# Optimization experiments

Measured on AMD Instinct MI355X. Metric: run time of the kernel, lower is better.

Reference implementation:

```python
import jax, jax.numpy as jnp
import numpy as np

# dims (match init_kwargs / input_specs)
B, T, IN, H, OUT, BR = 128, 250, 700, 512, 20, 4
VTH, DT, WARMUP = 1.0, 1.0, 10


@jax.custom_vjp
def spike_fn(v):
    # Heaviside spike with surrogate gradient (ActFun_adp style)
    return (v > 0.0).astype(v.dtype)

def _spike_fwd(v):
    return spike_fn(v), v

def _spike_bwd(v, g):
    gamma, lens = 0.5, 0.5  # gaussian surrogate
    return (g * gamma * jnp.exp(-v * v / (2.0 * lens * lens)),)

spike_fn.defvjp(_spike_fwd, _spike_bwd)


def make_mask(rng, out_dim, in_dim, branch):
    # each output neuron's branch j sees a disjoint random slice of inputs
    m = np.zeros((out_dim * branch, in_dim), np.float32)
    seg = in_dim // branch
    for i in range(out_dim):
        perm = rng.permutation(in_dim)
        for j in range(branch):
            m[i * branch + j, perm[j * seg:(j + 1) * seg]] = 1.0
    return jnp.asarray(m)


def setup_inputs() -> dict:
    key = jax.random.key(0)
    ks = jax.random.split(key, 12)
    rng = np.random.default_rng(0)
    lim1 = 1.0 / np.sqrt(IN)
    lim2 = 1.0 / np.sqrt(H)
    return {
        "x": jax.random.uniform(ks[0], (B, T, IN), dtype=jnp.float32),
        "W1": jax.random.uniform(ks[1], (H * BR, IN), minval=-lim1, maxval=lim1),
        "b1": jax.random.uniform(ks[2], (H * BR,), minval=-lim1, maxval=lim1),
        "tau_m1": jax.random.uniform(ks[3], (H,), minval=0.0, maxval=4.0),
        "tau_n1": jax.random.uniform(ks[4], (H, BR), minval=0.0, maxval=4.0),
        "mask1": make_mask(rng, H, IN, BR),
        "W2": jax.random.uniform(ks[5], (H * BR, H), minval=-lim2, maxval=lim2),
        "b2": jax.random.uniform(ks[6], (H * BR,), minval=-lim2, maxval=lim2),
        "tau_m2": jax.random.uniform(ks[7], (H,), minval=0.0, maxval=4.0),
        "tau_n2": jax.random.uniform(ks[8], (H, BR), minval=0.0, maxval=4.0),
        "mask2": make_mask(rng, H, H, BR),
        "Wo": jax.random.uniform(ks[9], (OUT, H), minval=-lim2, maxval=lim2),
        "bo": jax.random.uniform(ks[10], (OUT,), minval=-lim2, maxval=lim2),
        "tau_mo": jax.random.uniform(ks[11], (OUT,), minval=0.0, maxval=4.0),
    }


def reference(x, W1, b1, tau_m1, tau_n1, mask1, W2, b2, tau_m2, tau_n2, mask2, Wo, bo, tau_mo):
    beta1 = jax.nn.sigmoid(tau_n1)   # [H,BR] dendritic decay
    alpha1 = jax.nn.sigmoid(tau_m1)  # [H]   membrane decay
    beta2 = jax.nn.sigmoid(tau_n2)
    alpha2 = jax.nn.sigmoid(tau_m2)
    alpha_o = jax.nn.sigmoid(tau_mo)  # [OUT]
    Wm1 = W1 * mask1  # dendritic branch connectivity mask
    Wm2 = W2 * mask2
    Bsz = x.shape[0]
    Hd, Br = tau_n1.shape
    Od = tau_mo.shape[0]

    init = (jnp.zeros((Bsz, Hd, Br)), jnp.zeros((Bsz, Hd)), jnp.zeros((Bsz, Hd)),
            jnp.zeros((Bsz, Hd, Br)), jnp.zeros((Bsz, Hd)), jnp.zeros((Bsz, Hd)),
            jnp.zeros((Bsz, Od)))

    def step(c, xt):
        d1, m1, s1, d2, m2, s2, mo = c
        # layer 1: dendritic filter then LIF membrane with soft reset
        d1 = beta1 * d1 + (1.0 - beta1) * (xt @ Wm1.T + b1).reshape(Bsz, Hd, Br)
        m1 = m1 * alpha1 + (1.0 - alpha1) * DT * d1.sum(-1) - VTH * s1
        s1 = spike_fn(m1 - VTH)
        # layer 2
        d2 = beta2 * d2 + (1.0 - beta2) * (s1 @ Wm2.T + b2).reshape(Bsz, Hd, Br)
        m2 = m2 * alpha2 + (1.0 - alpha2) * DT * d2.sum(-1) - VTH * s2
        s2 = spike_fn(m2 - VTH)
        # leaky readout integrator (no spiking)
        mo = mo * alpha_o + (1.0 - alpha_o) * DT * (s2 @ Wo.T + bo)
        return (d1, m1, s1, d2, m2, s2, mo), jax.nn.softmax(mo, axis=1)

    _, ys = jax.lax.scan(step, init, jnp.swapaxes(x, 0, 1))  # ys: [T,B,OUT]
    # readout_mode == 'sum_softmax': skip steps i <= warmup_steps, sum the rest
    return ys[WARMUP + 1:].sum(0)
```

## Files before the change

### kernel.cpp

```cpp
#include <hip/hip_runtime.h>
#include <math.h>
#include <stdint.h>

#define B_    128
#define T_    250
#define IN_   700
#define INP_  704
#define H_    512
#define OUT_  20
#define BR_   4
#define HB_   2048
#define WARM_ 10
#define VTH_  1.0f

typedef __attribute__((ext_vector_type(8))) _Float16 half8;
typedef __attribute__((ext_vector_type(4))) float f32x4;
typedef __attribute__((ext_vector_type(4))) int i32x4;
typedef const __attribute__((address_space(1))) void* gptr_t;
typedef __attribute__((address_space(3))) void* lptr_t;

__global__ __launch_bounds__(256)
void w1prep_kernel(const float* __restrict__ W, const float* __restrict__ M,
                   _Float16* __restrict__ w0, _Float16* __restrict__ w1) {
    int i = blockIdx.x * 256 + threadIdx.x;
    if (i >= HB_ * INP_) return;
    int r = i / INP_, c = i - r * INP_;
    float v = (c < IN_) ? W[(size_t)r * IN_ + c] * M[(size_t)r * IN_ + c] : 0.f;
    _Float16 h0 = (_Float16)v;
    w0[i] = h0;
    w1[i] = (_Float16)(v - (float)h0);
}

__global__ __launch_bounds__(256)
void w2prep_kernel(const float* __restrict__ W, const float* __restrict__ M,
                   int8_t* __restrict__ p2, int8_t* __restrict__ p1,
                   int8_t* __restrict__ p0) {
    int i = blockIdx.x * 256 + threadIdx.x;
    if (i >= HB_ * H_) return;
    float v = W[i] * M[i];
    int q = (int)lrintf(v * 67108864.f);
    int b0 = (int)(int8_t)(q & 0xFF);  q = (q - b0) >> 8;
    int b1 = (int)(int8_t)(q & 0xFF);  int b2 = (q - b1) >> 8;
    p0[i] = (int8_t)b0; p1[i] = (int8_t)b1; p2[i] = (int8_t)b2;
}

__global__ __launch_bounds__(256)
void woprep_kernel(const float* __restrict__ Wo, _Float16* __restrict__ wo0,
                   _Float16* __restrict__ wo1) {
    int i = blockIdx.x * 256 + threadIdx.x;
    if (i >= 32 * H_) return;
    int n = i >> 9;
    float v = (n < OUT_) ? Wo[(size_t)n * H_ + (i & (H_ - 1))] : 0.f;
    _Float16 h0 = (_Float16)v;
    wo0[i] = h0;
    wo1[i] = (_Float16)(v - (float)h0);
}

__global__ __launch_bounds__(256)
void convx_kernel(const float* __restrict__ x, _Float16* __restrict__ x0,
                  _Float16* __restrict__ x1, int t0, int tc, int ntot) {
    int i = blockIdx.x * 256 + threadIdx.x;
    if (i >= ntot) return;
    int r = i / INP_, c = i - r * INP_;
    int bb = r / tc, tl = r - bb * tc;
    float v = (c < IN_) ? x[((size_t)bb * T_ + t0 + tl) * IN_ + c] : 0.f;
    _Float16 h0 = (_Float16)v;
    x0[i] = h0;
    x1[i] = (_Float16)(v - (float)h0);
}

__global__ void zero_kernel(float* __restrict__ p, int n4) {
    int i = blockIdx.x * blockDim.x + threadIdx.x;
    if (i < n4) ((float4*)p)[i] = make_float4(0.f, 0.f, 0.f, 0.f);
}

__global__ __launch_bounds__(256)
void l1_gemm_kernel(const _Float16* __restrict__ x0, const _Float16* __restrict__ x1,
                    const _Float16* __restrict__ w0, const _Float16* __restrict__ w1,
                    const float* __restrict__ bias, float* __restrict__ C) {
    __shared__ alignas(16) _Float16 A0s[128 * 32];
    __shared__ alignas(16) _Float16 A1s[128 * 32];
    __shared__ alignas(16) _Float16 B0s[128 * 32];
    __shared__ alignas(16) _Float16 B1s[128 * 32];
    const int tid  = threadIdx.x;
    const int wave = tid >> 6, lane = tid & 63;
    const int bm = blockIdx.x * 128, bn = blockIdx.y * 128;

    const int    srow  = tid >> 2;
    const int    skoff = (tid & 3) * 8;
    const size_t aoff0 = (size_t)(bm + srow) * INP_ + skoff;
    const size_t aoff1 = aoff0 + (size_t)64 * INP_;
    const size_t boff0 = (size_t)(bn + srow) * INP_ + skoff;
    const size_t boff1 = boff0 + (size_t)64 * INP_;
    const int lo0 = wave * 512, lo1 = 2048 + wave * 512;

    const int wm = wave & 1, wn = wave >> 1;
    const int fr = lane & 15;
    const int fk = (lane >> 4) * 8;

    f32x4 acc[4][4] = {};

    for (int kt = 0; kt < INP_ / 32; kt++) {
        const int k0 = kt * 32;
        __builtin_amdgcn_global_load_lds((gptr_t)(x0 + aoff0 + k0), (lptr_t)(A0s + lo0), 16, 0, 0);
        __builtin_amdgcn_global_load_lds((gptr_t)(x0 + aoff1 + k0), (lptr_t)(A0s + lo1), 16, 0, 0);
        __builtin_amdgcn_global_load_lds((gptr_t)(x1 + aoff0 + k0), (lptr_t)(A1s + lo0), 16, 0, 0);
        __builtin_amdgcn_global_load_lds((gptr_t)(x1 + aoff1 + k0), (lptr_t)(A1s + lo1), 16, 0, 0);
        __builtin_amdgcn_global_load_lds((gptr_t)(w0 + boff0 + k0), (lptr_t)(B0s + lo0), 16, 0, 0);
        __builtin_amdgcn_global_load_lds((gptr_t)(w0 + boff1 + k0), (lptr_t)(B0s + lo1), 16, 0, 0);
        __builtin_amdgcn_global_load_lds((gptr_t)(w1 + boff0 + k0), (lptr_t)(B1s + lo0), 16, 0, 0);
        __builtin_amdgcn_global_load_lds((gptr_t)(w1 + boff1 + k0), (lptr_t)(B1s + lo1), 16, 0, 0);
        __syncthreads();

        half8 a0[4], a1[4], b0[4], b1[4];
#pragma unroll
        for (int mi = 0; mi < 4; mi++)
            a0[mi] = *(const half8*)&A0s[(wm * 64 + mi * 16 + fr) * 32 + fk];
#pragma unroll
        for (int ni = 0; ni < 4; ni++)
            b0[ni] = *(const half8*)&B0s[(wn * 64 + ni * 16 + fr) * 32 + fk];
#pragma unroll
        for (int mi = 0; mi < 4; mi++)
#pragma unroll
            for (int ni = 0; ni < 4; ni++)
                acc[mi][ni] = __builtin_amdgcn_mfma_f32_16x16x32_f16(a0[mi], b0[ni], acc[mi][ni], 0, 0, 0);
#pragma unroll
        for (int ni = 0; ni < 4; ni++)
            b1[ni] = *(const half8*)&B1s[(wn * 64 + ni * 16 + fr) * 32 + fk];
#pragma unroll
        for (int mi = 0; mi < 4; mi++)
#pragma unroll
            for (int ni = 0; ni < 4; ni++)
                acc[mi][ni] = __builtin_amdgcn_mfma_f32_16x16x32_f16(a0[mi], b1[ni], acc[mi][ni], 0, 0, 0);
#pragma unroll
        for (int mi = 0; mi < 4; mi++)
            a1[mi] = *(const half8*)&A1s[(wm * 64 + mi * 16 + fr) * 32 + fk];
#pragma unroll
        for (int mi = 0; mi < 4; mi++)
#pragma unroll
            for (int ni = 0; ni < 4; ni++)
                acc[mi][ni] = __builtin_amdgcn_mfma_f32_16x16x32_f16(a1[mi], b0[ni], acc[mi][ni], 0, 0, 0);
        __syncthreads();
    }

    const int cc = lane & 15;
    const int cr = (lane >> 4) * 4;
#pragma unroll
    for (int ni = 0; ni < 4; ni++) {
        const int gc = bn + wn * 64 + ni * 16 + cc;
        const float bv = bias[gc];
#pragma unroll
        for (int mi = 0; mi < 4; mi++) {
            const int gr = bm + wm * 64 + mi * 16 + cr;
            float* cp = C + (size_t)gr * HB_ + gc;
#pragma unroll
            for (int r = 0; r < 4; r++) cp[(size_t)r * HB_] = acc[mi][ni][r] + bv;
        }
    }
}

__global__ __launch_bounds__(256)
void mfma_i8_gemm_kernel(const int8_t* __restrict__ A,
                         const int8_t* __restrict__ p2, const int8_t* __restrict__ p1,
                         const int8_t* __restrict__ p0,
                         const float* __restrict__ bias, float* __restrict__ C) {
    __shared__ alignas(16) int8_t As[128 * 64];
    __shared__ alignas(16) int8_t Bs[128 * 64];
    const int tid  = threadIdx.x;
    const int wave = tid >> 6, lane = tid & 63;
    const int bm = blockIdx.x * 128, bn = blockIdx.y * 128;

    const int    srow  = tid >> 2;
    const int    skoff = (tid & 3) * 16;
    const size_t aoff0 = (size_t)(bm + srow) * H_ + skoff;
    const size_t aoff1 = aoff0 + (size_t)64 * H_;
    const size_t boff0 = (size_t)(bn + srow) * H_ + skoff;
    const size_t boff1 = boff0 + (size_t)64 * H_;
    lptr_t lA0 = (lptr_t)(As + wave * 1024);
    lptr_t lA1 = (lptr_t)(As + 4096 + wave * 1024);
    lptr_t lB0 = (lptr_t)(Bs + wave * 1024);
    lptr_t lB1 = (lptr_t)(Bs + 4096 + wave * 1024);

    const int wm = wave & 1, wn = wave >> 1;
    const int fr = lane & 15;
    const int fk = (lane >> 4) * 16;

    const int8_t* planes[3] = {p2, p1, p0};
    i32x4 acc[4][4] = {};

#pragma unroll
    for (int s = 0; s < 3; s++) {
        if (s) {
#pragma unroll
            for (int mi = 0; mi < 4; mi++)
#pragma unroll
                for (int ni = 0; ni < 4; ni++) acc[mi][ni] *= 256;
        }
        const int8_t* pw = planes[s];
        for (int kt = 0; kt < H_ / 64; kt++) {
            const int k0 = kt * 64;
            __builtin_amdgcn_global_load_lds((gptr_t)(A  + aoff0 + k0), lA0, 16, 0, 0);
            __builtin_amdgcn_global_load_lds((gptr_t)(A  + aoff1 + k0), lA1, 16, 0, 0);
            __builtin_amdgcn_global_load_lds((gptr_t)(pw + boff0 + k0), lB0, 16, 0, 0);
            __builtin_amdgcn_global_load_lds((gptr_t)(pw + boff1 + k0), lB1, 16, 0, 0);
            __syncthreads();

            i32x4 af[4], bf[4];
#pragma unroll
            for (int mi = 0; mi < 4; mi++)
                af[mi] = *(const i32x4*)&As[(wm * 64 + mi * 16 + fr) * 64 + fk];
#pragma unroll
            for (int ni = 0; ni < 4; ni++)
                bf[ni] = *(const i32x4*)&Bs[(wn * 64 + ni * 16 + fr) * 64 + fk];
#pragma unroll
            for (int mi = 0; mi < 4; mi++)
#pragma unroll
                for (int ni = 0; ni < 4; ni++)
                    acc[mi][ni] = __builtin_amdgcn_mfma_i32_16x16x64_i8(
                        af[mi], bf[ni], acc[mi][ni], 0, 0, 0);
            __syncthreads();
        }
    }

    const float scale = 1.f / 67108864.f;
    const int cc = lane & 15;
    const int cr = (lane >> 4) * 4;
#pragma unroll
    for (int ni = 0; ni < 4; ni++) {
        const int gc = bn + wn * 64 + ni * 16 + cc;
        const float bv = bias[gc];
#pragma unroll
        for (int mi = 0; mi < 4; mi++) {
            const int gr = bm + wm * 64 + mi * 16 + cr;
            float* cp = C + (size_t)gr * HB_ + gc;
#pragma unroll
            for (int r = 0; r < 4; r++)
                cp[(size_t)r * HB_] = (float)acc[mi][ni][r] * scale + bv;
        }
    }
}

#define SCAN_BODY(SPIKE_STORE)                                                  \
    int idx = blockIdx.x * 256 + threadIdx.x;                                   \
    int b = idx >> 9;                                                           \
    int h = idx & (H_ - 1);                                                     \
    float alpha = 1.f / (1.f + expf(-tau_m[h]));                                \
    float4 tn = ((const float4*)tau_n)[h];                                      \
    float4 beta;                                                                \
    beta.x = 1.f / (1.f + expf(-tn.x));                                         \
    beta.y = 1.f / (1.f + expf(-tn.y));                                         \
    beta.z = 1.f / (1.f + expf(-tn.z));                                         \
    beta.w = 1.f / (1.f + expf(-tn.w));                                         \
    float4 d = ((const float4*)dst)[idx];                                       \
    float m = mst[idx];                                                         \
    float sp = spst[idx];                                                       \
    const float* cp = cur + (size_t)b * tc * HB_ + h * BR_;                     \
    for (int t = 0; t < tc; t++) {                                              \
        float4 c = *(const float4*)cp;                                          \
        cp += HB_;                                                              \
        d.x = beta.x * d.x + (1.f - beta.x) * c.x;                              \
        d.y = beta.y * d.y + (1.f - beta.y) * c.y;                              \
        d.z = beta.z * d.z + (1.f - beta.z) * c.z;                              \
        d.w = beta.w * d.w + (1.f - beta.w) * c.w;                              \
        float s4 = ((d.x + d.y) + d.z) + d.w;                                   \
        m = m * alpha + (1.f - alpha) * s4 - VTH_ * sp;                         \
        sp = (m > VTH_) ? 1.f : 0.f;                                            \
        SPIKE_STORE;                                                            \
    }                                                                           \
    ((float4*)dst)[idx] = d;                                                    \
    mst[idx] = m;                                                               \
    spst[idx] = sp;

__global__ __launch_bounds__(256)
void scan_i8_kernel(const float* __restrict__ cur, float* __restrict__ dst,
                    float* __restrict__ mst, float* __restrict__ spst,
                    int8_t* __restrict__ sout, const float* __restrict__ tau_m,
                    const float* __restrict__ tau_n, int tc) {
    SCAN_BODY(sout[((size_t)b * tc + t) * H_ + h] = (int8_t)(m > VTH_))
}

__global__ __launch_bounds__(256)
void scan_f16_kernel(const float* __restrict__ cur, float* __restrict__ dst,
                     float* __restrict__ mst, float* __restrict__ spst,
                     _Float16* __restrict__ sout, const float* __restrict__ tau_m,
                     const float* __restrict__ tau_n, int tc) {
    SCAN_BODY(sout[((size_t)b * tc + t) * H_ + h] = (_Float16)sp)
}

__global__ __launch_bounds__(256)
void rdot_mfma_kernel(const _Float16* __restrict__ s2c, const _Float16* __restrict__ wo0,
                      const _Float16* __restrict__ wo1, const float* __restrict__ bo,
                      float* __restrict__ curo, int t0, int tc) {
    __shared__ alignas(16) _Float16 As[128 * 32];
    __shared__ alignas(16) _Float16 B0s[32 * 32];
    __shared__ alignas(16) _Float16 B1s[32 * 32];
    const int tid  = threadIdx.x;
    const int wave = tid >> 6, lane = tid & 63;
    const int bm = blockIdx.x * 128;

    const int    srow  = tid >> 2;
    const int    skoff = (tid & 3) * 8;
    const size_t aoff0 = (size_t)(bm + srow) * H_ + skoff;
    const size_t aoff1 = aoff0 + (size_t)64 * H_;
    lptr_t lA0 = (lptr_t)(As + wave * 512);
    lptr_t lA1 = (lptr_t)(As + 2048 + wave * 512);
    const _Float16* bsrc = (wave < 2) ? wo0 : wo1;
    const int bw = wave & 1;
    const size_t boff = (size_t)(bw * 16 + (lane >> 2)) * H_ + (lane & 3) * 8;
    lptr_t lB = (lptr_t)(((wave < 2) ? B0s : B1s) + bw * 512);

    const int fr = lane & 15;
    const int fk = (lane >> 4) * 8;

    f32x4 acc[2][2] = {};

    for (int kt = 0; kt < H_ / 32; kt++) {
        const int k0 = kt * 32;
        __builtin_amdgcn_global_load_lds((gptr_t)(s2c + aoff0 + k0), lA0, 16, 0, 0);
        __builtin_amdgcn_global_load_lds((gptr_t)(s2c + aoff1 + k0), lA1, 16, 0, 0);
        __builtin_amdgcn_global_load_lds((gptr_t)(bsrc + boff + k0), lB, 16, 0, 0);
        __syncthreads();

        half8 af[2], b0[2], b1[2];
#pragma unroll
        for (int mi = 0; mi < 2; mi++)
            af[mi] = *(const half8*)&As[(wave * 32 + mi * 16 + fr) * 32 + fk];
#pragma unroll
        for (int ni = 0; ni < 2; ni++) {
            b0[ni] = *(const half8*)&B0s[(ni * 16 + fr) * 32 + fk];
            b1[ni] = *(const half8*)&B1s[(ni * 16 + fr) * 32 + fk];
        }
#pragma unroll
        for (int mi = 0; mi < 2; mi++)
#pragma unroll
            for (int ni = 0; ni < 2; ni++) {
                acc[mi][ni] = __builtin_amdgcn_mfma_f32_16x16x32_f16(af[mi], b0[ni], acc[mi][ni], 0, 0, 0);
                acc[mi][ni] = __builtin_amdgcn_mfma_f32_16x16x32_f16(af[mi], b1[ni], acc[mi][ni], 0, 0, 0);
            }
        __syncthreads();
    }

    const int cc = lane & 15;
    const int cr = (lane >> 4) * 4;
#pragma unroll
    for (int ni = 0; ni < 2; ni++) {
        const int gc = ni * 16 + cc;
        if (gc < OUT_) {
            const float bv = bo[gc];
#pragma unroll
            for (int mi = 0; mi < 2; mi++) {
#pragma unroll
                for (int r = 0; r < 4; r++) {
                    const int gr = bm + wave * 32 + mi * 16 + cr + r;
                    const int bb = gr / tc, tl = gr - bb * tc;
                    curo[((size_t)bb * T_ + t0 + tl) * OUT_ + gc] = acc[mi][ni][r] + bv;
                }
            }
        }
    }
}

#define RT_SEG 12
#define RT_LEN 21

__global__ __launch_bounds__(256)
void readout_kernel(const float* __restrict__ curo, const float* __restrict__ tau_mo,
                    float* __restrict__ out) {
    __shared__ float moS[T_ * OUT_];
    __shared__ float segA[RT_SEG][OUT_];
    __shared__ float segU[RT_SEG][OUT_];
    __shared__ float pre[RT_SEG][OUT_];
    __shared__ float accS[OUT_];
    const int b = blockIdx.x;
    const int tid = threadIdx.x;
    const float* cb = curo + (size_t)b * T_ * OUT_;

    const int o = tid % OUT_;
    const int sg = tid / OUT_;
    const float ao = 1.f / (1.f + expf(-tau_mo[o]));

    if (tid < RT_SEG * OUT_) {
        int t0 = sg * RT_LEN;
        int t1 = min(T_, t0 + RT_LEN);
        float u = 0.f, Ap = 1.f;
        for (int t = t0; t < t1; t++) {
            u = ao * u + (1.f - ao) * cb[t * OUT_ + o];
            Ap *= ao;
        }
        segU[sg][o] = u; segA[sg][o] = Ap;
    }
    if (tid < OUT_) accS[tid] = 0.f;
    __syncthreads();
    if (tid < OUT_) {
        float m = 0.f;
        for (int s = 0; s < RT_SEG; s++) {
            pre[s][tid] = m;
            m = segA[s][tid] * m + segU[s][tid];
        }
    }
    __syncthreads();
    if (tid < RT_SEG * OUT_) {
        int t0 = sg * RT_LEN;
        int t1 = min(T_, t0 + RT_LEN);
        float m = pre[sg][o];
        for (int t = t0; t < t1; t++) {
            m = ao * m + (1.f - ao) * cb[t * OUT_ + o];
            moS[t * OUT_ + o] = m;
        }
    }
    __syncthreads();
    if (tid >= WARM_ + 1 && tid < T_) {
        int t = tid;
        float mx = -3.0e38f;
#pragma unroll
        for (int o2 = 0; o2 < OUT_; o2++) mx = fmaxf(mx, moS[t * OUT_ + o2]);
        float es[OUT_]; float se = 0.f;
#pragma unroll
        for (int o2 = 0; o2 < OUT_; o2++) {
            float e = expf(moS[t * OUT_ + o2] - mx);
            es[o2] = e; se += e;
        }
        float inv = 1.f / se;
#pragma unroll
        for (int o2 = 0; o2 < OUT_; o2++) atomicAdd(&accS[o2], es[o2] * inv);
    }
    __syncthreads();
    if (tid < OUT_) out[(size_t)b * OUT_ + tid] = accS[tid];
}

extern "C" void kernel_launch(void* const* d_in, const int* in_sizes, int n_in,
                              void* d_out, int out_size, void* d_ws, size_t ws_size,
                              hipStream_t stream) {
    const float* x      = (const float*)d_in[0];
    const float* W1     = (const float*)d_in[1];
    const float* b1     = (const float*)d_in[2];
    const float* tau_m1 = (const float*)d_in[3];
    const float* tau_n1 = (const float*)d_in[4];
    const float* mask1  = (const float*)d_in[5];
    const float* W2     = (const float*)d_in[6];
    const float* b2     = (const float*)d_in[7];
    const float* tau_m2 = (const float*)d_in[8];
    const float* tau_n2 = (const float*)d_in[9];
    const float* mask2  = (const float*)d_in[10];
    const float* Wo     = (const float*)d_in[11];
    const float* bo     = (const float*)d_in[12];
    const float* tau_mo = (const float*)d_in[13];
    float* out = (float*)d_out;

    const size_t fixedB = (size_t)18 * 1024 * 1024;
    int ncs;  int tcs[3];
    if (ws_size >= fixedB + (size_t)250 * 1605632) { ncs = 1; tcs[0] = 250; }
    else if (ws_size >= fixedB + (size_t)125 * 1605632) { ncs = 2; tcs[0] = tcs[1] = 125; }
    else { ncs = 3; tcs[0] = 100; tcs[1] = 100; tcs[2] = 50; }
    const int tcm = tcs[0];

    char* p = (char*)d_ws;
    auto alloc = [&](size_t bytes) { char* r = p; p += (bytes + 255) & ~(size_t)255; return r; };
    _Float16* w10 = (_Float16*)alloc((size_t)HB_ * INP_ * 2);
    _Float16* w11 = (_Float16*)alloc((size_t)HB_ * INP_ * 2);
    int8_t*   q2  = (int8_t*)alloc((size_t)HB_ * H_);
    int8_t*   q1  = (int8_t*)alloc((size_t)HB_ * H_);
    int8_t*   q0  = (int8_t*)alloc((size_t)HB_ * H_);
    _Float16* wo0 = (_Float16*)alloc((size_t)32 * H_ * 2);
    _Float16* wo1 = (_Float16*)alloc((size_t)32 * H_ * 2);
    _Float16* xc0 = (_Float16*)alloc((size_t)B_ * tcm * INP_ * 2);
    _Float16* xc1 = (_Float16*)alloc((size_t)B_ * tcm * INP_ * 2);
    int8_t*   s1c = (int8_t*)alloc((size_t)B_ * tcm * H_);
    _Float16* s2c = (_Float16*)alloc((size_t)B_ * tcm * H_ * 2);
    float* cur    = (float*)alloc((size_t)B_ * tcm * HB_ * 4);
    float* curo   = (float*)alloc((size_t)B_ * T_ * OUT_ * 4);
    float* st     = (float*)alloc((size_t)786432 * 4);
    float* d1  = st;
    float* m1  = d1 + (size_t)B_ * H_ * BR_;
    float* sp1 = m1 + (size_t)B_ * H_;
    float* d2  = sp1 + (size_t)B_ * H_;
    float* m2  = d2 + (size_t)B_ * H_ * BR_;
    float* sp2 = m2 + (size_t)B_ * H_;

    w1prep_kernel<<<(HB_ * INP_ + 255) / 256, 256, 0, stream>>>(W1, mask1, w10, w11);
    w2prep_kernel<<<(HB_ * H_ + 255) / 256, 256, 0, stream>>>(W2, mask2, q2, q1, q0);
    woprep_kernel<<<(32 * H_ + 255) / 256, 256, 0, stream>>>(Wo, wo0, wo1);
    zero_kernel<<<(786432 / 4 + 255) / 256, 256, 0, stream>>>(st, 786432 / 4);

    int t0 = 0;
    for (int c = 0; c < ncs; c++) {
        const int tc = tcs[c];
        const int M = B_ * tc;
        dim3 gg(tc, HB_ / 128);
        convx_kernel<<<(M * INP_ + 255) / 256, 256, 0, stream>>>(x, xc0, xc1, t0, tc, M * INP_);
        l1_gemm_kernel<<<gg, 256, 0, stream>>>(xc0, xc1, w10, w11, b1, cur);
        scan_i8_kernel<<<B_ * H_ / 256, 256, 0, stream>>>(cur, d1, m1, sp1, s1c, tau_m1, tau_n1, tc);
        mfma_i8_gemm_kernel<<<gg, 256, 0, stream>>>(s1c, q2, q1, q0, b2, cur);
        scan_f16_kernel<<<B_ * H_ / 256, 256, 0, stream>>>(cur, d2, m2, sp2, s2c, tau_m2, tau_n2, tc);
        rdot_mfma_kernel<<<tc, 256, 0, stream>>>(s2c, wo0, wo1, bo, curo, t0, tc);
        t0 += tc;
    }
    readout_kernel<<<B_, 256, 0, stream>>>(curo, tau_mo, out);
}
```

Baseline: 925.5 us.

## Switch GEMMs to 32x32 MFMA tiles, swap grid order, alias spike buffers

Both the fp16 split-precision layer-1 GEMM and the int8 three-plane layer-2 GEMM move from 16x16 MFMA instructions to 32x32 ones (32x32x16 f16 and 32x32x32 i8). Each wave now holds a 2x2 grid of 16-register accumulators instead of 4x4 small ones, which is meant to cut instruction issue and LDS fragment reads per flop. The grid is transposed so the N dimension varies fastest, letting consecutive blocks share the same activation rows in cache. The workspace thresholds change, and in the single-chunk case the spike buffers reuse the converted-x buffers to save memory, which relies on those buffers no longer being needed at that point.

After: 851.8 us. 1.09x faster.

```diff
diff --git a/kernel.cpp b/kernel.cpp
--- a/kernel.cpp
+++ b/kernel.cpp
@@ -13,9 +13,11 @@
 #define WARM_ 10
 #define VTH_  1.0f
 
-typedef __attribute__((ext_vector_type(8))) _Float16 half8;
-typedef __attribute__((ext_vector_type(4))) float f32x4;
-typedef __attribute__((ext_vector_type(4))) int i32x4;
+typedef __attribute__((ext_vector_type(8)))  _Float16 half8;
+typedef __attribute__((ext_vector_type(4)))  float f32x4;
+typedef __attribute__((ext_vector_type(16))) float f32x16;
+typedef __attribute__((ext_vector_type(4)))  int i32x4;
+typedef __attribute__((ext_vector_type(16))) int i32x16;
 typedef const __attribute__((address_space(1))) void* gptr_t;
 typedef __attribute__((address_space(3))) void* lptr_t;
 
@@ -84,7 +86,7 @@
     __shared__ alignas(16) _Float16 B1s[128 * 32];
     const int tid  = threadIdx.x;
     const int wave = tid >> 6, lane = tid & 63;
-    const int bm = blockIdx.x * 128, bn = blockIdx.y * 128;
+    const int bm = blockIdx.y * 128, bn = blockIdx.x * 128;
 
     const int    srow  = tid >> 2;
     const int    skoff = (tid & 3) * 8;
@@ -95,10 +97,10 @@
     const int lo0 = wave * 512, lo1 = 2048 + wave * 512;
 
     const int wm = wave & 1, wn = wave >> 1;
-    const int fr = lane & 15;
-    const int fk = (lane >> 4) * 8;
-
-    f32x4 acc[4][4] = {};
+    const int row = lane & 31;
+    const int kh  = (lane >> 5) * 8;
+
+    f32x16 acc[2][2] = {};
 
     for (int kt = 0; kt < INP_ / 32; kt++) {
         const int k0 = kt * 32;
@@ -112,49 +114,67 @@
         __builtin_amdgcn_global_load_lds((gptr_t)(w1 + boff1 + k0), (lptr_t)(B1s + lo1), 16, 0, 0);
         __syncthreads();
 
-        half8 a0[4], a1[4], b0[4], b1[4];
-#pragma unroll
-        for (int mi = 0; mi < 4; mi++)
-            a0[mi] = *(const half8*)&A0s[(wm * 64 + mi * 16 + fr) * 32 + fk];
-#pragma unroll
-        for (int ni = 0; ni < 4; ni++)
-            b0[ni] = *(const half8*)&B0s[(wn * 64 + ni * 16 + fr) * 32 + fk];
-#pragma unroll
-        for (int mi = 0; mi < 4; mi++)
-#pragma unroll
-            for (int ni = 0; ni < 4; ni++)
-                acc[mi][ni] = __builtin_amdgcn_mfma_f32_16x16x32_f16(a0[mi], b0[ni], acc[mi][ni], 0, 0, 0);
-#pragma unroll
-        for (int ni = 0; ni < 4; ni++)
-            b1[ni] = *(const half8*)&B1s[(wn * 64 + ni * 16 + fr) * 32 + fk];
-#pragma unroll
-        for (int mi = 0; mi < 4; mi++)
-#pragma unroll
-            for (int ni = 0; ni < 4; ni++)
-                acc[mi][ni] = __builtin_amdgcn_mfma_f32_16x16x32_f16(a0[mi], b1[ni], acc[mi][ni], 0, 0, 0);
-#pragma unroll
-        for (int mi = 0; mi < 4; mi++)
-            a1[mi] = *(const half8*)&A1s[(wm * 64 + mi * 16 + fr) * 32 + fk];
-#pragma unroll
-        for (int mi = 0; mi < 4; mi++)
-#pragma unroll
-            for (int ni = 0; ni < 4; ni++)
-                acc[mi][ni] = __builtin_amdgcn_mfma_f32_16x16x32_f16(a1[mi], b0[ni], acc[mi][ni], 0, 0, 0);
+        half8 a0f[2][2], a1f[2][2], b0f[2][2], b1f[2][2];
+#pragma unroll
+        for (int mt = 0; mt < 2; mt++)
+#pragma unroll
+            for (int ks = 0; ks < 2; ks++)
+                a0f[mt][ks] = *(const half8*)&A0s[(wm * 64 + mt * 32 + row) * 32 + ks * 16 + kh];
+#pragma unroll
+        for (int nt = 0; nt < 2; nt++)
+#pragma unroll
+            for (int ks = 0; ks < 2; ks++)
+                b0f[nt][ks] = *(const half8*)&B0s[(wn * 64 + nt * 32 + row) * 32 + ks * 16 + kh];
+#pragma unroll
+        for (int ks = 0; ks < 2; ks++)
+#pragma unroll
+            for (int mt = 0; mt < 2; mt++)
+#pragma unroll
+                for (int nt = 0; nt < 2; nt++)
+                    acc[mt][nt] = __builtin_amdgcn_mfma_f32_32x32x16_f16(
+                        a0f[mt][ks], b0f[nt][ks], acc[mt][nt], 0, 0, 0);
+#pragma unroll
+        for (int nt = 0; nt < 2; nt++)
+#pragma unroll
+            for (int ks = 0; ks < 2; ks++)
+                b1f[nt][ks] = *(const half8*)&B1s[(wn * 64 + nt * 32 + row) * 32 + ks * 16 + kh];
+#pragma unroll
+        for (int ks = 0; ks < 2; ks++)
+#pragma unroll
+            for (int mt = 0; mt < 2; mt++)
+#pragma unroll
+                for (int nt = 0; nt < 2; nt++)
+                    acc[mt][nt] = __builtin_amdgcn_mfma_f32_32x32x16_f16(
+                        a0f[mt][ks], b1f[nt][ks], acc[mt][nt], 0, 0, 0);
+#pragma unroll
+        for (int mt = 0; mt < 2; mt++)
+#pragma unroll
+            for (int ks = 0; ks < 2; ks++)
+                a1f[mt][ks] = *(const half8*)&A1s[(wm * 64 + mt * 32 + row) * 32 + ks * 16 + kh];
+#pragma unroll
+        for (int ks = 0; ks < 2; ks++)
+#pragma unroll
+            for (int mt = 0; mt < 2; mt++)
+#pragma unroll
+                for (int nt = 0; nt < 2; nt++)
+                    acc[mt][nt] = __builtin_amdgcn_mfma_f32_32x32x16_f16(
+                        a1f[mt][ks], b0f[nt][ks], acc[mt][nt], 0, 0, 0);
         __syncthreads();
     }
 
-    const int cc = lane & 15;
-    const int cr = (lane >> 4) * 4;
-#pragma unroll
-    for (int ni = 0; ni < 4; ni++) {
-        const int gc = bn + wn * 64 + ni * 16 + cc;
+    const int col = lane & 31;
+    const int rb  = 4 * (lane >> 5);
+#pragma unroll
+    for (int nt = 0; nt < 2; nt++) {
+        const int gc = bn + wn * 64 + nt * 32 + col;
         const float bv = bias[gc];
 #pragma unroll
-        for (int mi = 0; mi < 4; mi++) {
-            const int gr = bm + wm * 64 + mi * 16 + cr;
-            float* cp = C + (size_t)gr * HB_ + gc;
-#pragma unroll
-            for (int r = 0; r < 4; r++) cp[(size_t)r * HB_] = acc[mi][ni][r] + bv;
+        for (int mt = 0; mt < 2; mt++) {
+#pragma unroll
+            for (int reg = 0; reg < 16; reg++) {
+                const int gr = bm + wm * 64 + mt * 32 + (reg & 3) + 8 * (reg >> 2) + rb;
+                C[(size_t)gr * HB_ + gc] = acc[mt][nt][reg] + bv;
+            }
         }
     }
 }
@@ -168,7 +188,7 @@
     __shared__ alignas(16) int8_t Bs[128 * 64];
     const int tid  = threadIdx.x;
     const int wave = tid >> 6, lane = tid & 63;
-    const int bm = blockIdx.x * 128, bn = blockIdx.y * 128;
+    const int bm = blockIdx.y * 128, bn = blockIdx.x * 128;
 
     const int    srow  = tid >> 2;
     const int    skoff = (tid & 3) * 16;
@@ -182,19 +202,19 @@
     lptr_t lB1 = (lptr_t)(Bs + 4096 + wave * 1024);
 
     const int wm = wave & 1, wn = wave >> 1;
-    const int fr = lane & 15;
-    const int fk = (lane >> 4) * 16;
+    const int row = lane & 31;
+    const int kb  = (lane >> 5) * 16;
 
     const int8_t* planes[3] = {p2, p1, p0};
-    i32x4 acc[4][4] = {};
+    i32x16 acc[2][2] = {};
 
 #pragma unroll
     for (int s = 0; s < 3; s++) {
         if (s) {
 #pragma unroll
-            for (int mi = 0; mi < 4; mi++)
-#pragma unroll
-                for (int ni = 0; ni < 4; ni++) acc[mi][ni] *= 256;
+            for (int mt = 0; mt < 2; mt++)
+#pragma unroll
+                for (int nt = 0; nt < 2; nt++) acc[mt][nt] *= 256;
         }
         const int8_t* pw = planes[s];
         for (int kt = 0; kt < H_ / 64; kt++) {
@@ -205,37 +225,43 @@
             __builtin_amdgcn_global_load_lds((gptr_t)(pw + boff1 + k0), lB1, 16, 0, 0);
             __syncthreads();
 
-            i32x4 af[4], bf[4];
-#pragma unroll
-            for (int mi = 0; mi < 4; mi++)
-                af[mi] = *(const i32x4*)&As[(wm * 64 + mi * 16 + fr) * 64 + fk];
-#pragma unroll
-            for (int ni = 0; ni < 4; ni++)
-                bf[ni] = *(const i32x4*)&Bs[(wn * 64 + ni * 16 + fr) * 64 + fk];
-#pragma unroll
-            for (int mi = 0; mi < 4; mi++)
-#pragma unroll
-                for (int ni = 0; ni < 4; ni++)
-                    acc[mi][ni] = __builtin_amdgcn_mfma_i32_16x16x64_i8(
-                        af[mi], bf[ni], acc[mi][ni], 0, 0, 0);
+            i32x4 af[2][2], bf[2][2];
+#pragma unroll
+            for (int mt = 0; mt < 2; mt++)
+#pragma unroll
+                for (int ks = 0; ks < 2; ks++)
+                    af[mt][ks] = *(const i32x4*)&As[(wm * 64 + mt * 32 + row) * 64 + ks * 32 + kb];
+#pragma unroll
+            for (int nt = 0; nt < 2; nt++)
+#pragma unroll
+                for (int ks = 0; ks < 2; ks++)
+                    bf[nt][ks] = *(const i32x4*)&Bs[(wn * 64 + nt * 32 + row) * 64 + ks * 32 + kb];
+#pragma unroll
+            for (int ks = 0; ks < 2; ks++)
+#pragma unroll
+                for (int mt = 0; mt < 2; mt++)
+#pragma unroll
+                    for (int nt = 0; nt < 2; nt++)
+                        acc[mt][nt] = __builtin_amdgcn_mfma_i32_32x32x32_i8(
+                            af[mt][ks], bf[nt][ks], acc[mt][nt], 0, 0, 0);
             __syncthreads();
         }
     }
 
     const float scale = 1.f / 67108864.f;
-    const int cc = lane & 15;
-    const int cr = (lane >> 4) * 4;
-#pragma unroll
-    for (int ni = 0; ni < 4; ni++) {
-        const int gc = bn + wn * 64 + ni * 16 + cc;
+    const int col = lane & 31;
+    const int rb  = 4 * (lane >> 5);
+#pragma unroll
+    for (int nt = 0; nt < 2; nt++) {
+        const int gc = bn + wn * 64 + nt * 32 + col;
         const float bv = bias[gc];
 #pragma unroll
-        for (int mi = 0; mi < 4; mi++) {
-            const int gr = bm + wm * 64 + mi * 16 + cr;
-            float* cp = C + (size_t)gr * HB_ + gc;
-#pragma unroll
-            for (int r = 0; r < 4; r++)
-                cp[(size_t)r * HB_] = (float)acc[mi][ni][r] * scale + bv;
+        for (int mt = 0; mt < 2; mt++) {
+#pragma unroll
+            for (int reg = 0; reg < 16; reg++) {
+                const int gr = bm + wm * 64 + mt * 32 + (reg & 3) + 8 * (reg >> 2) + rb;
+                C[(size_t)gr * HB_ + gc] = (float)acc[mt][nt][reg] * scale + bv;
+            }
         }
     }
 }
@@ -447,11 +473,11 @@
     const float* tau_mo = (const float*)d_in[13];
     float* out = (float*)d_out;
 
-    const size_t fixedB = (size_t)18 * 1024 * 1024;
     int ncs;  int tcs[3];
-    if (ws_size >= fixedB + (size_t)250 * 1605632) { ncs = 1; tcs[0] = 250; }
-    else if (ws_size >= fixedB + (size_t)125 * 1605632) { ncs = 2; tcs[0] = tcs[1] = 125; }
-    else { ncs = 3; tcs[0] = 100; tcs[1] = 100; tcs[2] = 50; }
+    bool single = (ws_size >= (size_t)368000000);
+    if (single)                                { ncs = 1; tcs[0] = 250; }
+    else if (ws_size >= (size_t)219000000)     { ncs = 2; tcs[0] = tcs[1] = 125; }
+    else                                       { ncs = 3; tcs[0] = 100; tcs[1] = 100; tcs[2] = 50; }
     const int tcm = tcs[0];
 
     char* p = (char*)d_ws;
@@ -465,8 +491,15 @@
     _Float16* wo1 = (_Float16*)alloc((size_t)32 * H_ * 2);
     _Float16* xc0 = (_Float16*)alloc((size_t)B_ * tcm * INP_ * 2);
     _Float16* xc1 = (_Float16*)alloc((size_t)B_ * tcm * INP_ * 2);
-    int8_t*   s1c = (int8_t*)alloc((size_t)B_ * tcm * H_);
-    _Float16* s2c = (_Float16*)alloc((size_t)B_ * tcm * H_ * 2);
+    int8_t*   s1c;
+    _Float16* s2c;
+    if (single) {
+        s1c = (int8_t*)xc0;
+        s2c = (_Float16*)xc1;
+    } else {
+        s1c = (int8_t*)alloc((size_t)B_ * tcm * H_);
+        s2c = (_Float16*)alloc((size_t)B_ * tcm * H_ * 2);
+    }
     float* cur    = (float*)alloc((size_t)B_ * tcm * HB_ * 4);
     float* curo   = (float*)alloc((size_t)B_ * T_ * OUT_ * 4);
     float* st     = (float*)alloc((size_t)786432 * 4);
@@ -486,13 +519,13 @@
     for (int c = 0; c < ncs; c++) {
         const int tc = tcs[c];
         const int M = B_ * tc;
-        dim3 gg(tc, HB_ / 128);
+        dim3 gg(HB_ / 128, M / 128);
         convx_kernel<<<(M * INP_ + 255) / 256, 256, 0, stream>>>(x, xc0, xc1, t0, tc, M * INP_);
         l1_gemm_kernel<<<gg, 256, 0, stream>>>(xc0, xc1, w10, w11, b1, cur);
         scan_i8_kernel<<<B_ * H_ / 256, 256, 0, stream>>>(cur, d1, m1, sp1, s1c, tau_m1, tau_n1, tc);
         mfma_i8_gemm_kernel<<<gg, 256, 0, stream>>>(s1c, q2, q1, q0, b2, cur);
         scan_f16_kernel<<<B_ * H_ / 256, 256, 0, stream>>>(cur, d2, m2, sp2, s2c, tau_m2, tau_n2, tc);
-        rdot_mfma_kernel<<<tc, 256, 0, stream>>>(s2c, wo0, wo1, bo, curo, t0, tc);
+        rdot_mfma_kernel<<<M / 128, 256, 0, stream>>>(s2c, wo0, wo1, bo, curo, t0, tc);
         t0 += tc;
     }
     readout_kernel<<<B_, 256, 0, stream>>>(curo, tau_mo, out);
```
